# Kernel tuning notes

Hardware: AMD Instinct MI355X
Metric: run time of the kernel (lower is better)

Reference implementation:

```python
import jax, jax.numpy as jnp
import numpy as np
import math

B, V, J, F, N = 32, 25000, 20, 50000, 200000
MIN_SCALE, MAX_SCALE = 5e-4, 0.05
INIT_SCALE = 0.005
EPS = 1e-8


def _normalize(x):
    return x / jnp.sqrt(jnp.sum(x * x, -1, keepdims=True) + 1e-12)


def _rodrigues(aa):
    # aa: [..., 3] axis-angle -> [..., 3, 3] rotation matrix
    theta = jnp.sqrt(jnp.sum(aa * aa, -1, keepdims=True) + 1e-12)
    axis = aa / theta
    x, y, z = axis[..., 0], axis[..., 1], axis[..., 2]
    zero = jnp.zeros_like(x)
    K = jnp.stack([zero, -z, y, z, zero, -x, -y, x, zero], -1).reshape(aa.shape[:-1] + (3, 3))
    s = jnp.sin(theta)[..., None]
    c = jnp.cos(theta)[..., None]
    I = jnp.eye(3, dtype=aa.dtype)
    return I + s * K + (1.0 - c) * (K @ K)


def _rt_to_mat4(R, t):
    top = jnp.concatenate([R, t[..., :, None]], axis=-1)  # [...,3,4]
    bot = jnp.broadcast_to(jnp.array([0.0, 0.0, 0.0, 1.0], R.dtype), top.shape[:-2] + (1, 4))
    return jnp.concatenate([top, bot], axis=-2)


def _rot_to_quat(R):
    # wxyz convention, branchless version of the torch masked code
    r00, r01, r02 = R[..., 0, 0], R[..., 0, 1], R[..., 0, 2]
    r10, r11, r12 = R[..., 1, 0], R[..., 1, 1], R[..., 1, 2]
    r20, r21, r22 = R[..., 2, 0], R[..., 2, 1], R[..., 2, 2]
    tr = r00 + r11 + r22
    s1 = jnp.sqrt(jnp.maximum(tr + 1.0, EPS)) * 2
    q1 = jnp.stack([0.25 * s1, (r21 - r12) / s1, (r02 - r20) / s1, (r10 - r01) / s1], -1)
    s2 = jnp.sqrt(jnp.maximum(1.0 + r00 - r11 - r22, EPS)) * 2
    q2 = jnp.stack([(r21 - r12) / s2, 0.25 * s2, (r01 + r10) / s2, (r02 + r20) / s2], -1)
    s3 = jnp.sqrt(jnp.maximum(1.0 + r11 - r00 - r22, EPS)) * 2
    q3 = jnp.stack([(r02 - r20) / s3, (r01 + r10) / s3, 0.25 * s3, (r12 + r21) / s3], -1)
    s4 = jnp.sqrt(jnp.maximum(1.0 + r22 - r00 - r11, EPS)) * 2
    q4 = jnp.stack([(r10 - r01) / s4, (r02 + r20) / s4, (r12 + r21) / s4, 0.25 * s4], -1)
    m1 = (tr > 0)[..., None]
    m2 = ((tr <= 0) & (r00 > r11) & (r00 > r22))[..., None]
    m3 = ((tr <= 0) & ~((r00 > r11) & (r00 > r22)) & (r11 > r22))[..., None]
    q = jnp.where(m1, q1, jnp.where(m2, q2, jnp.where(m3, q3, q4)))
    return _normalize(q)


def _quat_mul(a, b):
    # Hamilton product, wxyz
    w1, x1, y1, z1 = a[..., 0], a[..., 1], a[..., 2], a[..., 3]
    w2, x2, y2, z2 = b[..., 0], b[..., 1], b[..., 2], b[..., 3]
    return jnp.stack([
        w1 * w2 - x1 * x2 - y1 * y2 - z1 * z2,
        w1 * x2 + x1 * w2 + y1 * z2 - z1 * y2,
        w1 * y2 - x1 * z2 + y1 * w2 + z1 * x2,
        w1 * z2 + x1 * y2 - y1 * x2 + z1 * w2,
    ], -1)


def setup_inputs() -> dict:
    key = jax.random.key(0)
    ks = jax.random.split(key, 12)
    pose = 0.3 * jax.random.normal(ks[0], (B, J * 3), jnp.float32)
    trans = jax.random.normal(ks[1], (B, 3), jnp.float32)
    scale = 0.75 + 0.5 * jax.random.uniform(ks[2], (B, 1), jnp.float32)
    v_template = jax.random.normal(ks[3], (V, 3), jnp.float32)
    w = jax.random.uniform(ks[4], (V, J), jnp.float32) + 1e-3
    skin_weights = w / jnp.sum(w, -1, keepdims=True)
    joints_rest = jax.random.normal(ks[5], (J, 3), jnp.float32)
    position_offsets = 0.001 * jax.random.normal(ks[6], (N, 3), jnp.float32)
    colors_raw = 0.1 * jax.random.normal(ks[7], (N, 3), jnp.float32) - 1.7
    opacity_raw = jnp.full((N,), math.log(0.9 / 0.1), jnp.float32)
    log_scales = math.log(INIT_SCALE) + 0.1 * jax.random.normal(ks[8], (N, 3), jnp.float32)
    quaternions = jnp.concatenate(
        [jnp.ones((N, 1), jnp.float32), 0.01 * jax.random.normal(ks[9], (N, 3), jnp.float32)], -1)
    vertex_indices = jax.random.randint(ks[10], (N,), 0, V, jnp.int32)
    faces = jax.random.randint(ks[11], (F, 3), 0, V, jnp.int32)
    return dict(pose=pose, trans=trans, scale=scale, v_template=v_template,
                skin_weights=skin_weights, joints_rest=joints_rest,
                position_offsets=position_offsets, colors_raw=colors_raw,
                opacity_raw=opacity_raw, log_scales=log_scales,
                quaternions=quaternions, vertex_indices=vertex_indices, faces=faces)


def _lbs_vertices(pose, trans, scale, v_template, skin_weights, joints_rest):
    b = pose.shape[0]
    R = _rodrigues(pose.reshape(b, J, 3))  # [B,J,3,3]
    # kinematic chain: joint j's parent is j-1, joint 0 is root
    G = _rt_to_mat4(R[:, 0], jnp.broadcast_to(joints_rest[0], (b, 3)))
    Gs = [G]
    for j in range(1, J):
        L = _rt_to_mat4(R[:, j], jnp.broadcast_to(joints_rest[j] - joints_rest[j - 1], (b, 3)))
        G = G @ L
        Gs.append(G)
    G = jnp.stack(Gs, 1)  # [B,J,4,4]
    Rg = G[..., :3, :3]
    tg = G[..., :3, 3] - jnp.einsum('bjxy,jy->bjx', Rg, joints_rest)  # remove rest-pose joint
    A = _rt_to_mat4(Rg, tg)  # [B,J,4,4] relative transforms
    T = jnp.einsum('vj,bjxy->bvxy', skin_weights, A)  # blended per-vertex transform
    Vp = jnp.einsum('bvxy,vy->bvx', T[..., :3, :3], v_template) + T[..., :3, 3]
    return Vp * scale[:, None, :] + trans[:, None, :]  # [B,V,3]


def _tangent_frames(Vw, faces):
    fv = Vw[:, faces]  # [B,F,3,3]
    fn = jnp.cross(fv[:, :, 1] - fv[:, :, 0], fv[:, :, 2] - fv[:, :, 0])  # [B,F,3]
    nrm = jnp.zeros_like(Vw)
    for k in range(3):
        nrm = nrm.at[:, faces[:, k]].add(fn)
    n = _normalize(nrm)
    ref = jnp.where(jnp.abs(n[..., 0:1]) < 0.9,
                    jnp.array([1.0, 0.0, 0.0], n.dtype), jnp.array([0.0, 0.0, 1.0], n.dtype))
    t = _normalize(ref - jnp.sum(ref * n, -1, keepdims=True) * n)
    bt = jnp.cross(n, t)
    return n, t, bt


def reference(pose, trans, scale, v_template, skin_weights, joints_rest,
              position_offsets, colors_raw, opacity_raw, log_scales, quaternions,
              vertex_indices, faces):
    b = pose.shape[0]
    Vw = _lbs_vertices(pose, trans, scale, v_template, skin_weights, joints_rest)
    base = Vw[:, vertex_indices]  # [B,N,3] gather
    n, t, bt = _tangent_frames(Vw, faces)
    Ng = n[:, vertex_indices]
    Tg = t[:, vertex_indices]
    Bg = bt[:, vertex_indices]
    off = position_offsets[None]
    means = base + off[..., 0:1] * Tg + off[..., 1:2] * Bg + off[..., 2:3] * Ng
    frame = jnp.stack([Tg, Bg, Ng], axis=-1)  # [B,N,3,3] columns = T,B,N
    fq = _rot_to_quat(frame)
    lq = _normalize(quaternions)
    rotations = _quat_mul(fq, jnp.broadcast_to(lq[None], fq.shape))
    colors = jnp.broadcast_to(jax.nn.sigmoid(colors_raw)[None], (b, N, 3))
    opacity = jnp.broadcast_to(jax.nn.sigmoid(opacity_raw)[None], (b, N))
    scales = jnp.broadcast_to(jnp.clip(jnp.exp(log_scales), MIN_SCALE, MAX_SCALE)[None], (b, N, 3))
    return means, colors, opacity, scales, rotations
```

## Files before the change

### kernel.cpp

```cpp
#include <hip/hip_runtime.h>
#include <math.h>

namespace {
constexpr int kB = 32;
constexpr int kV = 25000;
constexpr int kJ = 20;
constexpr int kF = 50000;
constexpr int kN = 200000;
constexpr int kCap = 40;

constexpr float kEps = 1e-8f;

constexpr size_t OFF_MEANS  = 0;
constexpr size_t OFF_COLORS = (size_t)kB * kN * 3;
constexpr size_t OFF_OPAC   = OFF_COLORS + (size_t)kB * kN * 3;
constexpr size_t OFF_SCALE  = OFF_OPAC + (size_t)kB * kN;
constexpr size_t OFF_ROT    = OFF_SCALE + (size_t)kB * kN * 3;


constexpr size_t WS_A   = 0;
constexpr size_t WS_CNT = 32768;
constexpr size_t WS_TRI = 135168;
}

__global__ void fill_bucket_kernel(const int* __restrict__ faces,
                                   int* __restrict__ cursor,
                                   int4* __restrict__ tri) {
    int f = blockIdx.x * blockDim.x + threadIdx.x;
    if (f >= kF) return;
    int i0 = faces[f * 3 + 0];
    int i1 = faces[f * 3 + 1];
    int i2 = faces[f * 3 + 2];
    int4 rec = make_int4(i0, i1, i2, 0);
#pragma unroll
    for (int k = 0; k < 3; ++k) {
        int v = (k == 0) ? i0 : (k == 1) ? i1 : i2;
        int p = atomicAdd(&cursor[v], 1);
        if (p < kCap) tri[(size_t)p * kV + v] = rec;
    }
}

__global__ void jt_kernel(const float* __restrict__ pose,
                          const float* __restrict__ jr,
                          float* __restrict__ A) {
    int b = threadIdx.x;
    if (b >= kB) return;

    float Gr[9], Gt[3];
    for (int j = 0; j < kJ; ++j) {
        float ax = pose[b * (kJ * 3) + j * 3 + 0];
        float ay = pose[b * (kJ * 3) + j * 3 + 1];
        float az = pose[b * (kJ * 3) + j * 3 + 2];
        float t2 = ax * ax + ay * ay + az * az + 1e-12f;
        float th = sqrtf(t2);
        float inv = 1.0f / th;
        float ux = ax * inv, uy = ay * inv, uz = az * inv;
        float s = sinf(th), c = cosf(th), oc = 1.0f - c;
        float R[9];
        R[0] = 1.0f + oc * (-(uy * uy + uz * uz));
        R[1] = -s * uz + oc * (ux * uy);
        R[2] =  s * uy + oc * (ux * uz);
        R[3] =  s * uz + oc * (ux * uy);
        R[4] = 1.0f + oc * (-(ux * ux + uz * uz));
        R[5] = -s * ux + oc * (uy * uz);
        R[6] = -s * uy + oc * (ux * uz);
        R[7] =  s * ux + oc * (uy * uz);
        R[8] = 1.0f + oc * (-(ux * ux + uy * uy));

        float jx = jr[j * 3 + 0], jy = jr[j * 3 + 1], jz = jr[j * 3 + 2];

        if (j == 0) {
            for (int k = 0; k < 9; ++k) Gr[k] = R[k];
            Gt[0] = jx; Gt[1] = jy; Gt[2] = jz;
        } else {
            float pjx = jr[(j - 1) * 3 + 0];
            float pjy = jr[(j - 1) * 3 + 1];
            float pjz = jr[(j - 1) * 3 + 2];
            float ltx = jx - pjx, lty = jy - pjy, ltz = jz - pjz;
            float nR[9], nT[3];
            for (int r = 0; r < 3; ++r) {
                float g0 = Gr[r * 3 + 0], g1 = Gr[r * 3 + 1], g2 = Gr[r * 3 + 2];
                nR[r * 3 + 0] = g0 * R[0] + g1 * R[3] + g2 * R[6];
                nR[r * 3 + 1] = g0 * R[1] + g1 * R[4] + g2 * R[7];
                nR[r * 3 + 2] = g0 * R[2] + g1 * R[5] + g2 * R[8];
                nT[r] = g0 * ltx + g1 * lty + g2 * ltz + Gt[r];
            }
            for (int k = 0; k < 9; ++k) Gr[k] = nR[k];
            Gt[0] = nT[0]; Gt[1] = nT[1]; Gt[2] = nT[2];
        }

        float tgx = Gt[0] - (Gr[0] * jx + Gr[1] * jy + Gr[2] * jz);
        float tgy = Gt[1] - (Gr[3] * jx + Gr[4] * jy + Gr[5] * jz);
        float tgz = Gt[2] - (Gr[6] * jx + Gr[7] * jy + Gr[8] * jz);
        float* Ao = A + ((size_t)b * kJ + j) * 12;
        Ao[0] = Gr[0]; Ao[1] = Gr[1]; Ao[2]  = Gr[2]; Ao[3]  = tgx;
        Ao[4] = Gr[3]; Ao[5] = Gr[4]; Ao[6]  = Gr[5]; Ao[7]  = tgy;
        Ao[8] = Gr[6]; Ao[9] = Gr[7]; Ao[10] = Gr[8]; Ao[11] = tgz;
    }
}

__global__ void skin_kernel(const float* __restrict__ A,
                            const float* __restrict__ sw,
                            const float* __restrict__ vt,
                            const float* __restrict__ scale,
                            const float* __restrict__ trans,
                            float4* __restrict__ Vw) {
    int b = blockIdx.x;
    int v = blockIdx.y * blockDim.x + threadIdx.x;
    __shared__ float sA[kJ * 12];
    if (threadIdx.x < kJ * 12) sA[threadIdx.x] = A[(size_t)b * kJ * 12 + threadIdx.x];
    __syncthreads();
    if (v >= kV) return;

    const float4* sw4 = (const float4*)(sw + (size_t)v * kJ);
    float w[kJ];
#pragma unroll
    for (int q = 0; q < 5; ++q) {
        float4 f = sw4[q];
        w[q * 4 + 0] = f.x; w[q * 4 + 1] = f.y;
        w[q * 4 + 2] = f.z; w[q * 4 + 3] = f.w;
    }

    float T[12];
#pragma unroll
    for (int k = 0; k < 12; ++k) T[k] = 0.0f;
#pragma unroll
    for (int j = 0; j < kJ; ++j) {
        float wj = w[j];
#pragma unroll
        for (int k = 0; k < 12; ++k) T[k] += wj * sA[j * 12 + k];
    }
    float x = vt[v * 3 + 0], y = vt[v * 3 + 1], z = vt[v * 3 + 2];
    float px = T[0] * x + T[1] * y + T[2]  * z + T[3];
    float py = T[4] * x + T[5] * y + T[6]  * z + T[7];
    float pz = T[8] * x + T[9] * y + T[10] * z + T[11];
    float s = scale[b];
    float tx = trans[b * 3 + 0], ty = trans[b * 3 + 1], tz = trans[b * 3 + 2];
    Vw[(size_t)b * kV + v] = make_float4(px * s + tx, py * s + ty, pz * s + tz, 0.0f);
}

__global__ void frame_kernel(const float4* __restrict__ Vw,
                             const int* __restrict__ cnt,
                             const int4* __restrict__ tri,
                             float4* __restrict__ rec) {
    int b = blockIdx.x;
    int v = blockIdx.y * blockDim.x + threadIdx.x;
    if (v >= kV) return;
    const float4* base = Vw + (size_t)b * kV;
    float4 me = base[v];

    int deg = min(cnt[v], kCap);
    float sx = 0.0f, sy = 0.0f, sz = 0.0f;
    for (int i = 0; i < deg; ++i) {
        int4 t = tri[(size_t)i * kV + v];
        float4 a  = base[t.x];
        float4 c1 = base[t.y];
        float4 c2 = base[t.z];
        float e1x = c1.x - a.x, e1y = c1.y - a.y, e1z = c1.z - a.z;
        float e2x = c2.x - a.x, e2y = c2.y - a.y, e2z = c2.z - a.z;
        sx += e1y * e2z - e1z * e2y;
        sy += e1z * e2x - e1x * e2z;
        sz += e1x * e2y - e1y * e2x;
    }

    float ninv = rsqrtf(sx * sx + sy * sy + sz * sz + 1e-12f);
    float nx = sx * ninv, ny = sy * ninv, nz = sz * ninv;

    bool small = fabsf(nx) < 0.9f;
    float refx = small ? 1.0f : 0.0f;
    float refz = small ? 0.0f : 1.0f;
    float d = refx * nx + refz * nz;
    float tx0 = refx - d * nx, ty0 = -d * ny, tz0 = refz - d * nz;
    float tinv = rsqrtf(tx0 * tx0 + ty0 * ty0 + tz0 * tz0 + 1e-12f);
    float tx = tx0 * tinv, ty = ty0 * tinv, tz = tz0 * tinv;

    float btx = ny * tz - nz * ty;
    float bty = nz * tx - nx * tz;
    float btz = nx * ty - ny * tx;

    float r00 = tx, r01 = btx, r02 = nx;
    float r10 = ty, r11 = bty, r12 = ny;
    float r20 = tz, r21 = btz, r22 = nz;
    float tr = r00 + r11 + r22;
    float q0, q1, q2, q3;
    if (tr > 0.0f) {
        float s = sqrtf(fmaxf(tr + 1.0f, kEps)) * 2.0f;
        q0 = 0.25f * s;
        q1 = (r21 - r12) / s;
        q2 = (r02 - r20) / s;
        q3 = (r10 - r01) / s;
    } else if (r00 > r11 && r00 > r22) {
        float s = sqrtf(fmaxf(1.0f + r00 - r11 - r22, kEps)) * 2.0f;
        q0 = (r21 - r12) / s;
        q1 = 0.25f * s;
        q2 = (r01 + r10) / s;
        q3 = (r02 + r20) / s;
    } else if (r11 > r22) {
        float s = sqrtf(fmaxf(1.0f + r11 - r00 - r22, kEps)) * 2.0f;
        q0 = (r02 - r20) / s;
        q1 = (r01 + r10) / s;
        q2 = 0.25f * s;
        q3 = (r12 + r21) / s;
    } else {
        float s = sqrtf(fmaxf(1.0f + r22 - r00 - r11, kEps)) * 2.0f;
        q0 = (r10 - r01) / s;
        q1 = (r02 + r20) / s;
        q2 = (r12 + r21) / s;
        q3 = 0.25f * s;
    }
    float qinv = rsqrtf(q0 * q0 + q1 * q1 + q2 * q2 + q3 * q3 + 1e-12f);
    q0 *= qinv; q1 *= qinv; q2 *= qinv; q3 *= qinv;

    size_t ro = ((size_t)b * kV + v) * 2;
    rec[ro + 0] = make_float4(me.x, me.y, me.z, 0.0f);
    rec[ro + 1] = make_float4(q0, q1, q2, q3);
}

__global__ void finalize_mr4_kernel(const float4* __restrict__ rec,
                                    const int* __restrict__ vidx,
                                    const float* __restrict__ poff,
                                    const float* __restrict__ quat,
                                    float* __restrict__ out) {
    int b = blockIdx.x;
    int qi = blockIdx.y * blockDim.x + threadIdx.x;
    if (qi >= kN / 4) return;
    int n0 = qi * 4;

    int4 vi = *(const int4*)(vidx + n0);
    const float4* rb = rec + (size_t)b * kV * 2;

    float4 p[4], fq[4];
    p[0] = rb[(size_t)vi.x * 2]; fq[0] = rb[(size_t)vi.x * 2 + 1];
    p[1] = rb[(size_t)vi.y * 2]; fq[1] = rb[(size_t)vi.y * 2 + 1];
    p[2] = rb[(size_t)vi.z * 2]; fq[2] = rb[(size_t)vi.z * 2 + 1];
    p[3] = rb[(size_t)vi.w * 2]; fq[3] = rb[(size_t)vi.w * 2 + 1];

    const float4* po = (const float4*)(poff + (size_t)n0 * 3);
    float4 oa = po[0], ob = po[1], oc = po[2];
    float off[4][3] = {{oa.x, oa.y, oa.z}, {oa.w, ob.x, ob.y},
                       {ob.z, ob.w, oc.x}, {oc.y, oc.z, oc.w}};

    const float4* lq4 = (const float4*)(quat + (size_t)n0 * 4);

    float m[4][3];
    float4 rotv[4];
#pragma unroll
    for (int k = 0; k < 4; ++k) {
        float w = fq[k].x, x = fq[k].y, y = fq[k].z, z = fq[k].w;
        float tx = 1.0f - 2.0f * (y * y + z * z);
        float ty = 2.0f * (x * y + w * z);
        float tz = 2.0f * (x * z - w * y);
        float btx = 2.0f * (x * y - w * z);
        float bty = 1.0f - 2.0f * (x * x + z * z);
        float btz = 2.0f * (y * z + w * x);
        float nx = 2.0f * (x * z + w * y);
        float ny = 2.0f * (y * z - w * x);
        float nz = 1.0f - 2.0f * (x * x + y * y);

        float o0 = off[k][0], o1 = off[k][1], o2 = off[k][2];
        m[k][0] = p[k].x + o0 * tx + o1 * btx + o2 * nx;
        m[k][1] = p[k].y + o0 * ty + o1 * bty + o2 * ny;
        m[k][2] = p[k].z + o0 * tz + o1 * btz + o2 * nz;

        float4 lq = lq4[k];
        float lw = lq.x, lx = lq.y, ly = lq.z, lz = lq.w;
        float linv = rsqrtf(lw * lw + lx * lx + ly * ly + lz * lz + 1e-12f);
        lw *= linv; lx *= linv; ly *= linv; lz *= linv;

        rotv[k] = make_float4(w * lw - x * lx - y * ly - z * lz,
                              w * lx + x * lw + y * lz - z * ly,
                              w * ly - x * lz + y * lw + z * lx,
                              w * lz + x * ly - y * lx + z * lw);
    }

    size_t bn0 = (size_t)b * kN + n0;
    float4* mo = (float4*)(out + OFF_MEANS + bn0 * 3);
    mo[0] = make_float4(m[0][0], m[0][1], m[0][2], m[1][0]);
    mo[1] = make_float4(m[1][1], m[1][2], m[2][0], m[2][1]);
    mo[2] = make_float4(m[2][2], m[3][0], m[3][1], m[3][2]);
    float4* ro = (float4*)(out + OFF_ROT + bn0 * 4);
    ro[0] = rotv[0]; ro[1] = rotv[1]; ro[2] = rotv[2]; ro[3] = rotv[3];
}

__device__ __forceinline__ float sigm(float x) {
    return 1.0f / (1.0f + __expf(-x));
}
__device__ __forceinline__ float eclip(float x) {
    return fminf(fmaxf(__expf(x), 0.0005f), 0.05f);
}

__global__ void finalize_cos_kernel(const float* __restrict__ craw,
                                    const float* __restrict__ oraw,
                                    const float* __restrict__ lsc,
                                    float* __restrict__ out) {
    int b = blockIdx.x;
    int q = blockIdx.y * blockDim.x + threadIdx.x;
    if (q >= kN / 4) return;
    int n0 = q * 4;

    const float4* cr4 = (const float4*)(craw + (size_t)n0 * 3);
    float4 ca = cr4[0], cb = cr4[1], cc = cr4[2];
    float4 ov = *(const float4*)(oraw + n0);
    const float4* ls4 = (const float4*)(lsc + (size_t)n0 * 3);
    float4 la = ls4[0], lb = ls4[1], lc = ls4[2];

    float4 sa = make_float4(sigm(ca.x), sigm(ca.y), sigm(ca.z), sigm(ca.w));
    float4 sb = make_float4(sigm(cb.x), sigm(cb.y), sigm(cb.z), sigm(cb.w));
    float4 sc = make_float4(sigm(cc.x), sigm(cc.y), sigm(cc.z), sigm(cc.w));
    float4 so = make_float4(sigm(ov.x), sigm(ov.y), sigm(ov.z), sigm(ov.w));
    float4 ea = make_float4(eclip(la.x), eclip(la.y), eclip(la.z), eclip(la.w));
    float4 eb = make_float4(eclip(lb.x), eclip(lb.y), eclip(lb.z), eclip(lb.w));
    float4 ec = make_float4(eclip(lc.x), eclip(lc.y), eclip(lc.z), eclip(lc.w));

    size_t bn0 = (size_t)b * kN + n0;
    float4* co = (float4*)(out + OFF_COLORS + bn0 * 3);
    co[0] = sa; co[1] = sb; co[2] = sc;
    *(float4*)(out + OFF_OPAC + bn0) = so;
    float4* sco = (float4*)(out + OFF_SCALE + bn0 * 3);
    sco[0] = ea; sco[1] = eb; sco[2] = ec;
}

extern "C" void kernel_launch(void* const* d_in, const int* in_sizes, int n_in,
                              void* d_out, int out_size, void* d_ws, size_t ws_size,
                              hipStream_t stream) {
    const float* pose  = (const float*)d_in[0];
    const float* trans = (const float*)d_in[1];
    const float* scale = (const float*)d_in[2];
    const float* vt    = (const float*)d_in[3];
    const float* sw    = (const float*)d_in[4];
    const float* jr    = (const float*)d_in[5];
    const float* poff  = (const float*)d_in[6];
    const float* craw  = (const float*)d_in[7];
    const float* oraw  = (const float*)d_in[8];
    const float* lsc   = (const float*)d_in[9];
    const float* quat  = (const float*)d_in[10];
    const int*   vidx  = (const int*)d_in[11];
    const int*   faces = (const int*)d_in[12];
    float* out = (float*)d_out;
    char* ws = (char*)d_ws;

    float* A   = (float*)(ws + WS_A);
    int*   cnt = (int*)(ws + WS_CNT);
    int4*  tri = (int4*)(ws + WS_TRI);

    float4* rec = (float4*)(out + OFF_OPAC);
    float4* Vw  = (float4*)(out + OFF_SCALE);

    dim3 gV(kB, (kV + 255) / 256);
    dim3 gQ(kB, (kN / 4 + 255) / 256);

    hipMemsetAsync(cnt, 0, kV * sizeof(int), stream);
    fill_bucket_kernel<<<(kF + 255) / 256, 256, 0, stream>>>(faces, cnt, tri);

    jt_kernel<<<1, 64, 0, stream>>>(pose, jr, A);
    skin_kernel<<<gV, 256, 0, stream>>>(A, sw, vt, scale, trans, Vw);

    frame_kernel<<<gV, 256, 0, stream>>>(Vw, cnt, tri, rec);

    finalize_mr4_kernel<<<gQ, 256, 0, stream>>>(rec, vidx, poff, quat, out);

    finalize_cos_kernel<<<gQ, 256, 0, stream>>>(craw, oraw, lsc, out);
}
```

Before: 284.6 us.

## Pack triangle records, fuse setup kernels, use nontemporal stores, batch cos outputs

Merges the face-bucket fill and joint-transform kernels into one launch. Replaces each 16-byte per-vertex triangle record with a packed 32-bit word holding the two other vertex indices (15 bits each) and the slot position, which cuts bucket traffic in the frame kernel. Switches the large output writes to nontemporal stores and has each finalize_cos thread write two batches, halving its input reads and its launch grid. The 15-bit packing assumes vertex indices stay below 32768, which holds for V=25000 but is fragile.

Result: slower. 316.8 us (+11.3%).

```diff
diff --git a/kernel.cpp b/kernel.cpp
--- a/kernel.cpp
+++ b/kernel.cpp
@@ -23,26 +23,43 @@
 constexpr size_t WS_TRI = 135168;
 }
 
-__global__ void fill_bucket_kernel(const int* __restrict__ faces,
-                                   int* __restrict__ cursor,
-                                   int4* __restrict__ tri) {
-    int f = blockIdx.x * blockDim.x + threadIdx.x;
-    if (f >= kF) return;
-    int i0 = faces[f * 3 + 0];
-    int i1 = faces[f * 3 + 1];
-    int i2 = faces[f * 3 + 2];
-    int4 rec = make_int4(i0, i1, i2, 0);
-#pragma unroll
-    for (int k = 0; k < 3; ++k) {
-        int v = (k == 0) ? i0 : (k == 1) ? i1 : i2;
-        int p = atomicAdd(&cursor[v], 1);
-        if (p < kCap) tri[(size_t)p * kV + v] = rec;
-    }
-}
-
-__global__ void jt_kernel(const float* __restrict__ pose,
-                          const float* __restrict__ jr,
-                          float* __restrict__ A) {
+typedef float f4 __attribute__((ext_vector_type(4)));
+
+__device__ __forceinline__ void nt_store4(float* p, float a, float b,
+                                          float c, float d) {
+    f4 v = {a, b, c, d};
+    __builtin_nontemporal_store(v, (f4*)p);
+}
+__device__ __forceinline__ void nt_store4v(float* p, float4 v) {
+    nt_store4(p, v.x, v.y, v.z, v.w);
+}
+
+__global__ void fill_jt_kernel(const int* __restrict__ faces,
+                               int* __restrict__ cursor,
+                               unsigned int* __restrict__ tri,
+                               const float* __restrict__ pose,
+                               const float* __restrict__ jr,
+                               float* __restrict__ A,
+                               int nf_blocks) {
+    if ((int)blockIdx.x < nf_blocks) {
+        int f = blockIdx.x * blockDim.x + threadIdx.x;
+        if (f >= kF) return;
+        int i0 = faces[f * 3 + 0];
+        int i1 = faces[f * 3 + 1];
+        int i2 = faces[f * 3 + 2];
+        const int vs[3] = {i0, i1, i2};
+#pragma unroll
+        for (int k = 0; k < 3; ++k) {
+            int v = vs[k];
+            unsigned int ia = (k == 0) ? (unsigned)i1 : (unsigned)i0;
+            unsigned int ib = (k == 2) ? (unsigned)i1 : (unsigned)i2;
+            unsigned int rec = ia | (ib << 15) | ((unsigned)k << 30);
+            int p = atomicAdd(&cursor[v], 1);
+            if (p < kCap) tri[(size_t)p * kV + v] = rec;
+        }
+        return;
+    }
+
     int b = threadIdx.x;
     if (b >= kB) return;
 
@@ -141,7 +158,7 @@
 
 __global__ void frame_kernel(const float4* __restrict__ Vw,
                              const int* __restrict__ cnt,
-                             const int4* __restrict__ tri,
+                             const unsigned int* __restrict__ tri,
                              float4* __restrict__ rec) {
     int b = blockIdx.x;
     int v = blockIdx.y * blockDim.x + threadIdx.x;
@@ -152,10 +169,16 @@
     int deg = min(cnt[v], kCap);
     float sx = 0.0f, sy = 0.0f, sz = 0.0f;
     for (int i = 0; i < deg; ++i) {
-        int4 t = tri[(size_t)i * kV + v];
-        float4 a  = base[t.x];
-        float4 c1 = base[t.y];
-        float4 c2 = base[t.z];
+        unsigned int r = tri[(size_t)i * kV + v];
+        int ia = (int)(r & 0x7fffu);
+        int ib = (int)((r >> 15) & 0x7fffu);
+        int k  = (int)(r >> 30);
+        int i0 = (k == 0) ? v : ia;
+        int i1 = (k == 0) ? ia : ((k == 1) ? v : ib);
+        int i2 = (k == 2) ? v : ib;
+        float4 a  = base[i0];
+        float4 c1 = base[i1];
+        float4 c2 = base[i2];
         float e1x = c1.x - a.x, e1y = c1.y - a.y, e1z = c1.z - a.z;
         float e2x = c2.x - a.x, e2y = c2.y - a.y, e2z = c2.z - a.z;
         sx += e1y * e2z - e1z * e2y;
@@ -274,12 +297,15 @@
     }
 
     size_t bn0 = (size_t)b * kN + n0;
-    float4* mo = (float4*)(out + OFF_MEANS + bn0 * 3);
-    mo[0] = make_float4(m[0][0], m[0][1], m[0][2], m[1][0]);
-    mo[1] = make_float4(m[1][1], m[1][2], m[2][0], m[2][1]);
-    mo[2] = make_float4(m[2][2], m[3][0], m[3][1], m[3][2]);
-    float4* ro = (float4*)(out + OFF_ROT + bn0 * 4);
-    ro[0] = rotv[0]; ro[1] = rotv[1]; ro[2] = rotv[2]; ro[3] = rotv[3];
+    float* mo = out + OFF_MEANS + bn0 * 3;
+    nt_store4(mo + 0, m[0][0], m[0][1], m[0][2], m[1][0]);
+    nt_store4(mo + 4, m[1][1], m[1][2], m[2][0], m[2][1]);
+    nt_store4(mo + 8, m[2][2], m[3][0], m[3][1], m[3][2]);
+    float* ro = out + OFF_ROT + bn0 * 4;
+    nt_store4v(ro + 0,  rotv[0]);
+    nt_store4v(ro + 4,  rotv[1]);
+    nt_store4v(ro + 8,  rotv[2]);
+    nt_store4v(ro + 12, rotv[3]);
 }
 
 __device__ __forceinline__ float sigm(float x) {
@@ -293,7 +319,7 @@
                                     const float* __restrict__ oraw,
                                     const float* __restrict__ lsc,
                                     float* __restrict__ out) {
-    int b = blockIdx.x;
+    int b0 = blockIdx.x * 2;
     int q = blockIdx.y * blockDim.x + threadIdx.x;
     if (q >= kN / 4) return;
     int n0 = q * 4;
@@ -312,12 +338,19 @@
     float4 eb = make_float4(eclip(lb.x), eclip(lb.y), eclip(lb.z), eclip(lb.w));
     float4 ec = make_float4(eclip(lc.x), eclip(lc.y), eclip(lc.z), eclip(lc.w));
 
-    size_t bn0 = (size_t)b * kN + n0;
-    float4* co = (float4*)(out + OFF_COLORS + bn0 * 3);
-    co[0] = sa; co[1] = sb; co[2] = sc;
-    *(float4*)(out + OFF_OPAC + bn0) = so;
-    float4* sco = (float4*)(out + OFF_SCALE + bn0 * 3);
-    sco[0] = ea; sco[1] = eb; sco[2] = ec;
+#pragma unroll
+    for (int g = 0; g < 2; ++g) {
+        size_t bn0 = (size_t)(b0 + g) * kN + n0;
+        float* co = out + OFF_COLORS + bn0 * 3;
+        nt_store4v(co + 0, sa);
+        nt_store4v(co + 4, sb);
+        nt_store4v(co + 8, sc);
+        nt_store4v(out + OFF_OPAC + bn0, so);
+        float* sco = out + OFF_SCALE + bn0 * 3;
+        nt_store4v(sco + 0, ea);
+        nt_store4v(sco + 4, eb);
+        nt_store4v(sco + 8, ec);
+    }
 }
 
 extern "C" void kernel_launch(void* const* d_in, const int* in_sizes, int n_in,
@@ -339,25 +372,24 @@
     float* out = (float*)d_out;
     char* ws = (char*)d_ws;
 
-    float* A   = (float*)(ws + WS_A);
-    int*   cnt = (int*)(ws + WS_CNT);
-    int4*  tri = (int4*)(ws + WS_TRI);
+    float*        A   = (float*)(ws + WS_A);
+    int*          cnt = (int*)(ws + WS_CNT);
+    unsigned int* tri = (unsigned int*)(ws + WS_TRI);
 
     float4* rec = (float4*)(out + OFF_OPAC);
     float4* Vw  = (float4*)(out + OFF_SCALE);
 
     dim3 gV(kB, (kV + 255) / 256);
     dim3 gQ(kB, (kN / 4 + 255) / 256);
-
-    hipMemsetAsync(cnt, 0, kV * sizeof(int), stream);
-    fill_bucket_kernel<<<(kF + 255) / 256, 256, 0, stream>>>(faces, cnt, tri);
-
-    jt_kernel<<<1, 64, 0, stream>>>(pose, jr, A);
+    dim3 gC(kB / 2, (kN / 4 + 255) / 256);
+
+    int nf_blocks = (kF + 255) / 256;
+    (void)hipMemsetAsync(cnt, 0, kV * sizeof(int), stream);
+    fill_jt_kernel<<<nf_blocks + 1, 256, 0, stream>>>(faces, cnt, tri,
+                                                      pose, jr, A, nf_blocks);
+
     skin_kernel<<<gV, 256, 0, stream>>>(A, sw, vt, scale, trans, Vw);
-
     frame_kernel<<<gV, 256, 0, stream>>>(Vw, cnt, tri, rec);
-
     finalize_mr4_kernel<<<gQ, 256, 0, stream>>>(rec, vidx, poff, quat, out);
-
-    finalize_cos_kernel<<<gQ, 256, 0, stream>>>(craw, oraw, lsc, out);
-}
+    finalize_cos_kernel<<<gC, 256, 0, stream>>>(craw, oraw, lsc, out);
+}
```
